# Kernel tuning notes

Measured on AMD Instinct MI355X. Metric: run time of the kernel, lower is better.

Reference implementation:

```python
import jax, jax.numpy as jnp
import numpy as np

QMIN, QMAX = -128.0, 127.0

def setup_inputs() -> dict:
    key = jax.random.key(0)
    kA, kB, ksA, ksB, kso = jax.random.split(key, 5)
    M, K, N = 8192, 4096, 4096
    # int8-valued operands (stored as int32 for portability)
    A = jax.random.randint(kA, (M, K), -128, 128, dtype=jnp.int32)
    B = jax.random.randint(kB, (N, K), -128, 128, dtype=jnp.int32)
    # strictly positive scales, typical quantization magnitudes
    scale_A = jax.random.uniform(ksA, (M,), dtype=jnp.float32, minval=0.005, maxval=0.02)
    scale_B = jax.random.uniform(ksB, (N,), dtype=jnp.float32, minval=0.005, maxval=0.02)
    scale_out = jax.random.uniform(kso, (M,), dtype=jnp.float32, minval=0.05, maxval=0.5)
    return {"A": A, "scale_A": scale_A, "B": B, "scale_B": scale_B, "scale_out": scale_out}

def reference(A, scale_A, B, scale_B, scale_out):
    # int8 GEMM with int32 accumulation: C = A @ B^T, shape (M, N)
    acc = jax.lax.dot_general(
        A, B, (((1,), (1,)), ((), ())), preferred_element_type=jnp.int32
    ).astype(jnp.float32)
    # fused three-scale dequant/requant epilogue:
    #   C_fp = acc * scale_A[m] * scale_B[n]; C_int8 = round(C_fp / scale_out[m])
    x = acc * (scale_A / scale_out)[:, None] * scale_B[None, :]
    C_int8 = jnp.clip(jnp.round(x), QMIN, QMAX).astype(jnp.int8)
    return C_int8, scale_out
```

## Files before the change

kernel.cpp:

```cpp
#include <hip/hip_runtime.h>
#include <hip/hip_bf16.h>
#include <stdint.h>

#define M_DIM 8192
#define K_DIM 4096
#define N_DIM 4096

#define BM 128
#define BN 128
#define BK 64

typedef int v4i __attribute__((ext_vector_type(4)));

__global__ void convert_pack_kernel(const int* __restrict__ A,
                                    const int* __restrict__ B,
                                    const float* __restrict__ scale_out,
                                    int8_t* __restrict__ A8,
                                    int8_t* __restrict__ B8,
                                    float* __restrict__ out_tail) {
  long gid = blockIdx.x * (long)blockDim.x + threadIdx.x;
  long stride = (long)gridDim.x * blockDim.x;

  for (long i = gid; i < M_DIM; i += stride) out_tail[i] = scale_out[i];

  const long agran = (long)M_DIM * K_DIM / 16;
  const long total = (long)(M_DIM + N_DIM) * K_DIM / 16;
  for (long g = gid; g < total; g += stride) {
    const int4* src;
    int4* dst;
    if (g < agran) {
      src = ((const int4*)A) + g * 4;
      dst = ((int4*)A8) + g;
    } else {
      long h = g - agran;
      src = ((const int4*)B) + h * 4;
      dst = ((int4*)B8) + h;
    }
    int4 a = src[0], b = src[1], c = src[2], d = src[3];
    int4 o;
    o.x = (a.x & 255) | ((a.y & 255) << 8) | ((a.z & 255) << 16) | ((a.w & 255) << 24);
    o.y = (b.x & 255) | ((b.y & 255) << 8) | ((b.z & 255) << 16) | ((b.w & 255) << 24);
    o.z = (c.x & 255) | ((c.y & 255) << 8) | ((c.z & 255) << 16) | ((c.w & 255) << 24);
    o.w = (d.x & 255) | ((d.y & 255) << 8) | ((d.z & 255) << 16) | ((d.w & 255) << 24);
    dst[0] = o;
  }
}

__global__ __launch_bounds__(256) void gemm_i8_kernel(
    const int8_t* __restrict__ A8, const int8_t* __restrict__ B8,
    const float* __restrict__ sA, const float* __restrict__ sB,
    const float* __restrict__ sO, float* __restrict__ out) {
  __shared__ int8_t lA[BM * BK];
  __shared__ int8_t lB[BN * BK];

  const int tid = threadIdx.x;
  const int wid = tid >> 6;
  const int lane = tid & 63;

  const int nwg = gridDim.x;
  const int cpx = nwg >> 3;
  const int bid = blockIdx.x;
  const int wg = (bid & 7) * cpx + (bid >> 3);
  const int tm = wg >> 5;
  const int tn = wg & 31;
  const int row0 = tm * BM;
  const int col0 = tn * BN;

  const int j = lane;
  const int koff = (((j & 3) ^ ((j >> 3) & 3)) << 4);
  const int r_lo = 16 * wid + (j >> 2);
  const int r_hi = r_lo + 64;

  const int8_t* pA0 = A8 + (size_t)(row0 + r_lo) * K_DIM + koff;
  const int8_t* pA1 = A8 + (size_t)(row0 + r_hi) * K_DIM + koff;
  const int8_t* pB0 = B8 + (size_t)(col0 + r_lo) * K_DIM + koff;
  const int8_t* pB1 = B8 + (size_t)(col0 + r_hi) * K_DIM + koff;

  int8_t* dA0 = lA + wid * 1024;
  int8_t* dA1 = lA + (wid + 4) * 1024;
  int8_t* dB0 = lB + wid * 1024;
  int8_t* dB1 = lB + (wid + 4) * 1024;

  const int fr = lane & 15;
  const int fk = lane >> 4;
  const int wr = wid >> 1;
  const int wc = wid & 1;

  int aoff[4], boff[4];
#pragma unroll
  for (int m = 0; m < 4; ++m) {
    int r = wr * 64 + m * 16 + fr;
    aoff[m] = (r * 4 + (fk ^ ((r >> 1) & 3))) * 16;
  }
#pragma unroll
  for (int n = 0; n < 4; ++n) {
    int r = wc * 64 + n * 16 + fr;
    boff[n] = (r * 4 + (fk ^ ((r >> 1) & 3))) * 16;
  }

  v4i acc[4][4];
#pragma unroll
  for (int m = 0; m < 4; ++m)
#pragma unroll
    for (int n = 0; n < 4; ++n) acc[m][n] = (v4i){0, 0, 0, 0};

  const int KSTEPS = K_DIM / BK;
  for (int kt = 0; kt < KSTEPS; ++kt) {
    __builtin_amdgcn_global_load_lds(
        (const __attribute__((address_space(1))) void*)pA0,
        (__attribute__((address_space(3))) void*)dA0, 16, 0, 0);
    __builtin_amdgcn_global_load_lds(
        (const __attribute__((address_space(1))) void*)pA1,
        (__attribute__((address_space(3))) void*)dA1, 16, 0, 0);
    __builtin_amdgcn_global_load_lds(
        (const __attribute__((address_space(1))) void*)pB0,
        (__attribute__((address_space(3))) void*)dB0, 16, 0, 0);
    __builtin_amdgcn_global_load_lds(
        (const __attribute__((address_space(1))) void*)pB1,
        (__attribute__((address_space(3))) void*)dB1, 16, 0, 0);
    pA0 += BK; pA1 += BK; pB0 += BK; pB1 += BK;

    __syncthreads();

    v4i a[4], b[4];
#pragma unroll
    for (int m = 0; m < 4; ++m) a[m] = *(const v4i*)(lA + aoff[m]);
#pragma unroll
    for (int n = 0; n < 4; ++n) b[n] = *(const v4i*)(lB + boff[n]);

#pragma unroll
    for (int m = 0; m < 4; ++m)
#pragma unroll
      for (int n = 0; n < 4; ++n)
        acc[m][n] = __builtin_amdgcn_mfma_i32_16x16x64_i8(a[m], b[n],
                                                          acc[m][n], 0, 0, 0);

    __syncthreads();
  }

  const int orow = row0 + wr * 64;
  const int ocol = col0 + wc * 64;

  float sbv[4];
#pragma unroll
  for (int n = 0; n < 4; ++n) sbv[n] = sB[ocol + n * 16 + fr];

#pragma unroll
  for (int m = 0; m < 4; ++m) {
#pragma unroll
    for (int reg = 0; reg < 4; ++reg) {
      const int grow = orow + m * 16 + fk * 4 + reg;
      const float rA = sA[grow] / sO[grow];
#pragma unroll
      for (int n = 0; n < 4; ++n) {
        float f = rintf(((float)acc[m][n][reg] * rA) * sbv[n]);
        f = fminf(127.0f, fmaxf(-128.0f, f));
        out[(size_t)grow * N_DIM + (ocol + n * 16 + fr)] = f;
      }
    }
  }
}

__global__ void gemm_naive_kernel(const int* __restrict__ A,
                                  const int* __restrict__ B,
                                  const float* __restrict__ sA,
                                  const float* __restrict__ sB,
                                  const float* __restrict__ sO,
                                  float* __restrict__ out) {
  long idx = blockIdx.x * (long)blockDim.x + threadIdx.x;
  if (idx >= (long)M_DIM * N_DIM) return;
  int m = (int)(idx / N_DIM);
  int n = (int)(idx % N_DIM);
  const int4* a = (const int4*)(A + (size_t)m * K_DIM);
  const int4* b = (const int4*)(B + (size_t)n * K_DIM);
  int acc = 0;
  for (int k = 0; k < K_DIM / 4; ++k) {
    int4 x = a[k], y = b[k];
    acc += x.x * y.x + x.y * y.y + x.z * y.z + x.w * y.w;
  }
  float f = rintf((float)acc * (sA[m] / sO[m]) * sB[n]);
  out[idx] = fminf(127.0f, fmaxf(-128.0f, f));
}

__global__ void tail_copy_kernel(const float* __restrict__ scale_out,
                                 float* __restrict__ out_tail) {
  int i = blockIdx.x * blockDim.x + threadIdx.x;
  if (i < M_DIM) out_tail[i] = scale_out[i];
}

extern "C" void kernel_launch(void* const* d_in, const int* in_sizes, int n_in,
                              void* d_out, int out_size, void* d_ws,
                              size_t ws_size, hipStream_t stream) {
  const int* A = (const int*)d_in[0];
  const float* sA = (const float*)d_in[1];
  const int* B = (const int*)d_in[2];
  const float* sB = (const float*)d_in[3];
  const float* sO = (const float*)d_in[4];
  float* out = (float*)d_out;
  float* out_tail = out + (size_t)M_DIM * N_DIM;

  const size_t need = (size_t)(M_DIM + N_DIM) * K_DIM;
  if (ws_size >= need) {
    int8_t* A8 = (int8_t*)d_ws;
    int8_t* B8 = A8 + (size_t)M_DIM * K_DIM;
    convert_pack_kernel<<<2048, 256, 0, stream>>>(A, B, sO, A8, B8, out_tail);
    gemm_i8_kernel<<<2048, 256, 0, stream>>>(A8, B8, sA, sB, sO, out);
  } else {
    tail_copy_kernel<<<(M_DIM + 255) / 256, 256, 0, stream>>>(sO, out_tail);
    long total = (long)M_DIM * N_DIM;
    int blocks = (int)((total + 255) / 256);
    gemm_naive_kernel<<<blocks, 256, 0, stream>>>(A, B, sA, sB, sO, out);
  }
}
```

Measured before the change: 470.1 us.

## Rewrite int8 GEMM as 256x256 tile, 8-wave, double-buffered phased pipeline

Replaces the 128x128x64 single-buffered GEMM with a 256x256x128 tile computed by 8 waves. The K loop runs as four phases that interleave LDS reads, async global-to-LDS staging of the next tile and MFMA bursts, with explicit barriers, waitcnt and setprio. The A/sO ratio is precomputed in the pack kernel, and packing switches to per-int4 conversion. The aim is to hide global load latency and raise data reuse per LDS byte. The cost is 128KB of LDS and a large accumulator register file, which limits occupancy to one block per CU.

After: 395.6 us. 15.9% less time.

```diff
diff --git a/kernel.cpp b/kernel.cpp
--- a/kernel.cpp
+++ b/kernel.cpp
@@ -5,157 +5,204 @@
 #define M_DIM 8192
 #define K_DIM 4096
 #define N_DIM 4096
-
-#define BM 128
-#define BN 128
-#define BK 64
+#define NT (K_DIM / 128)
 
 typedef int v4i __attribute__((ext_vector_type(4)));
 
 __global__ void convert_pack_kernel(const int* __restrict__ A,
                                     const int* __restrict__ B,
-                                    const float* __restrict__ scale_out,
-                                    int8_t* __restrict__ A8,
-                                    int8_t* __restrict__ B8,
+                                    const float* __restrict__ sA,
+                                    const float* __restrict__ sO,
+                                    int* __restrict__ A8, int* __restrict__ B8,
+                                    float* __restrict__ rAs,
                                     float* __restrict__ out_tail) {
   long gid = blockIdx.x * (long)blockDim.x + threadIdx.x;
   long stride = (long)gridDim.x * blockDim.x;
 
-  for (long i = gid; i < M_DIM; i += stride) out_tail[i] = scale_out[i];
-
-  const long agran = (long)M_DIM * K_DIM / 16;
-  const long total = (long)(M_DIM + N_DIM) * K_DIM / 16;
-  for (long g = gid; g < total; g += stride) {
-    const int4* src;
-    int4* dst;
-    if (g < agran) {
-      src = ((const int4*)A) + g * 4;
-      dst = ((int4*)A8) + g;
-    } else {
-      long h = g - agran;
-      src = ((const int4*)B) + h * 4;
-      dst = ((int4*)B8) + h;
-    }
-    int4 a = src[0], b = src[1], c = src[2], d = src[3];
-    int4 o;
-    o.x = (a.x & 255) | ((a.y & 255) << 8) | ((a.z & 255) << 16) | ((a.w & 255) << 24);
-    o.y = (b.x & 255) | ((b.y & 255) << 8) | ((b.z & 255) << 16) | ((b.w & 255) << 24);
-    o.z = (c.x & 255) | ((c.y & 255) << 8) | ((c.z & 255) << 16) | ((c.w & 255) << 24);
-    o.w = (d.x & 255) | ((d.y & 255) << 8) | ((d.z & 255) << 16) | ((d.w & 255) << 24);
-    dst[0] = o;
-  }
-}
-
-__global__ __launch_bounds__(256) void gemm_i8_kernel(
+  for (long i = gid; i < M_DIM; i += stride) {
+    float so = sO[i];
+    out_tail[i] = so;
+    rAs[i] = sA[i] / so;
+  }
+
+  const long MK4 = (long)M_DIM * (K_DIM / 4);
+  for (long i = gid; i < MK4; i += stride) {
+    int4 v = ((const int4*)A)[i];
+    A8[i] = (v.x & 255) | ((v.y & 255) << 8) | ((v.z & 255) << 16) |
+            ((v.w & 255) << 24);
+  }
+  const long NK4 = (long)N_DIM * (K_DIM / 4);
+  for (long i = gid; i < NK4; i += stride) {
+    int4 v = ((const int4*)B)[i];
+    B8[i] = (v.x & 255) | ((v.y & 255) << 8) | ((v.z & 255) << 16) |
+            ((v.w & 255) << 24);
+  }
+}
+
+__device__ __forceinline__ void stage_half(const int8_t* g, int8_t* smdst,
+                                           int rowoff, int t) {
+  const int tt = (t < NT) ? t : (NT - 1);
+  const int8_t* s = g + rowoff * K_DIM + tt * 128;
+  __builtin_amdgcn_global_load_lds(
+      (const __attribute__((address_space(1))) void*)s,
+      (__attribute__((address_space(3))) void*)smdst, 16, 0, 0);
+  __builtin_amdgcn_global_load_lds(
+      (const __attribute__((address_space(1))) void*)(s + 8 * K_DIM),
+      (__attribute__((address_space(3))) void*)(smdst + 1024), 16, 0, 0);
+}
+
+__device__ __forceinline__ void read_a4(const int8_t* smc, int ar0, int mb,
+                                        v4i a[4][2]) {
+#pragma unroll
+  for (int mm = 0; mm < 4; ++mm) {
+    a[mm][0] = *(const v4i*)(smc + (ar0 + (mb + mm) * 2048));
+    a[mm][1] = *(const v4i*)(smc + ((ar0 + (mb + mm) * 2048) ^ 64));
+  }
+}
+
+__device__ __forceinline__ void read_b2(const int8_t* smc, int br0, int nb0,
+                                        v4i b[4][2]) {
+#pragma unroll
+  for (int nn = 0; nn < 2; ++nn) {
+    b[nb0 + nn][0] = *(const v4i*)(smc + (br0 + (nb0 + nn) * 2048));
+    b[nb0 + nn][1] = *(const v4i*)(smc + ((br0 + (nb0 + nn) * 2048) ^ 64));
+  }
+}
+
+__device__ __forceinline__ void mfma16(v4i a[4][2], v4i b[4][2], v4i acc[8][4],
+                                       int am, int bn) {
+#pragma unroll
+  for (int s = 0; s < 2; ++s)
+#pragma unroll
+    for (int mm = 0; mm < 4; ++mm)
+#pragma unroll
+      for (int nn = 0; nn < 2; ++nn)
+        acc[am + mm][bn + nn] = __builtin_amdgcn_mfma_i32_16x16x64_i8(
+            a[mm][s], b[bn + nn][s], acc[am + mm][bn + nn], 0, 0, 0);
+}
+
+#define BAR() __builtin_amdgcn_s_barrier()
+#define LGKM0()                                         \
+  {                                                     \
+    asm volatile("s_waitcnt lgkmcnt(0)" ::: "memory"); \
+    __builtin_amdgcn_sched_barrier(0);                  \
+  }
+#define VM2() asm volatile("s_waitcnt vmcnt(2)" ::: "memory")
+#define SP(x) __builtin_amdgcn_s_setprio(x)
+
+__global__ __launch_bounds__(512) void gemm_i8_8phase(
     const int8_t* __restrict__ A8, const int8_t* __restrict__ B8,
-    const float* __restrict__ sA, const float* __restrict__ sB,
-    const float* __restrict__ sO, float* __restrict__ out) {
-  __shared__ int8_t lA[BM * BK];
-  __shared__ int8_t lB[BN * BK];
+    const float* __restrict__ rAs, const float* __restrict__ sB,
+    float* __restrict__ out) {
+  __shared__ int8_t sm[2][65536];
 
   const int tid = threadIdx.x;
   const int wid = tid >> 6;
-  const int lane = tid & 63;
-
-  const int nwg = gridDim.x;
-  const int cpx = nwg >> 3;
+  const int l = tid & 63;
+
   const int bid = blockIdx.x;
-  const int wg = (bid & 7) * cpx + (bid >> 3);
-  const int tm = wg >> 5;
-  const int tn = wg & 31;
-  const int row0 = tm * BM;
-  const int col0 = tn * BN;
-
-  const int j = lane;
-  const int koff = (((j & 3) ^ ((j >> 3) & 3)) << 4);
-  const int r_lo = 16 * wid + (j >> 2);
-  const int r_hi = r_lo + 64;
-
-  const int8_t* pA0 = A8 + (size_t)(row0 + r_lo) * K_DIM + koff;
-  const int8_t* pA1 = A8 + (size_t)(row0 + r_hi) * K_DIM + koff;
-  const int8_t* pB0 = B8 + (size_t)(col0 + r_lo) * K_DIM + koff;
-  const int8_t* pB1 = B8 + (size_t)(col0 + r_hi) * K_DIM + koff;
-
-  int8_t* dA0 = lA + wid * 1024;
-  int8_t* dA1 = lA + (wid + 4) * 1024;
-  int8_t* dB0 = lB + wid * 1024;
-  int8_t* dB1 = lB + (wid + 4) * 1024;
-
-  const int fr = lane & 15;
-  const int fk = lane >> 4;
-  const int wr = wid >> 1;
-  const int wc = wid & 1;
-
-  int aoff[4], boff[4];
-#pragma unroll
-  for (int m = 0; m < 4; ++m) {
-    int r = wr * 64 + m * 16 + fr;
-    aoff[m] = (r * 4 + (fk ^ ((r >> 1) & 3))) * 16;
-  }
-#pragma unroll
-  for (int n = 0; n < 4; ++n) {
-    int r = wc * 64 + n * 16 + fr;
-    boff[n] = (r * 4 + (fk ^ ((r >> 1) & 3))) * 16;
-  }
-
-  v4i acc[4][4];
-#pragma unroll
-  for (int m = 0; m < 4; ++m)
-#pragma unroll
-    for (int n = 0; n < 4; ++n) acc[m][n] = (v4i){0, 0, 0, 0};
-
-  const int KSTEPS = K_DIM / BK;
-  for (int kt = 0; kt < KSTEPS; ++kt) {
-    __builtin_amdgcn_global_load_lds(
-        (const __attribute__((address_space(1))) void*)pA0,
-        (__attribute__((address_space(3))) void*)dA0, 16, 0, 0);
-    __builtin_amdgcn_global_load_lds(
-        (const __attribute__((address_space(1))) void*)pA1,
-        (__attribute__((address_space(3))) void*)dA1, 16, 0, 0);
-    __builtin_amdgcn_global_load_lds(
-        (const __attribute__((address_space(1))) void*)pB0,
-        (__attribute__((address_space(3))) void*)dB0, 16, 0, 0);
-    __builtin_amdgcn_global_load_lds(
-        (const __attribute__((address_space(1))) void*)pB1,
-        (__attribute__((address_space(3))) void*)dB1, 16, 0, 0);
-    pA0 += BK; pA1 += BK; pB0 += BK; pB1 += BK;
-
-    __syncthreads();
-
-    v4i a[4], b[4];
-#pragma unroll
-    for (int m = 0; m < 4; ++m) a[m] = *(const v4i*)(lA + aoff[m]);
-#pragma unroll
-    for (int n = 0; n < 4; ++n) b[n] = *(const v4i*)(lB + boff[n]);
-
-#pragma unroll
-    for (int m = 0; m < 4; ++m)
-#pragma unroll
-      for (int n = 0; n < 4; ++n)
-        acc[m][n] = __builtin_amdgcn_mfma_i32_16x16x64_i8(a[m], b[n],
-                                                          acc[m][n], 0, 0, 0);
-
-    __syncthreads();
-  }
-
-  const int orow = row0 + wr * 64;
+  const int wg = (bid & 7) * (512 / 8) + (bid >> 3);
+  const int tm = wg >> 4;
+  const int tn = wg & 15;
+  const int row0 = tm * 256;
+  const int col0 = tn * 256;
+
+  const int srcChunk = ((l & 7) ^ (l >> 3)) << 4;
+  const int rowLane = l >> 3;
+  const int8_t* gA = A8 + (size_t)(row0 + rowLane) * K_DIM + srcChunk;
+  const int8_t* gB = B8 + (size_t)(col0 + rowLane) * K_DIM + srcChunk;
+
+  const int wr = wid >> 2;
+  const int wc = wid & 3;
+  const int fr = l & 15;
+  const int fk = l >> 4;
+  const int ar0 = (wr * 128 + fr) * 128 + ((fk ^ (l & 3)) << 4) +
+                  (((l >> 2) & 1) << 6);
+  const int br0 = 32768 + (wc * 64 + fr) * 128 + ((fk ^ (l & 3)) << 4) +
+                  (((l >> 2) & 1) << 6);
+
+  v4i a[4][2], b[4][2];
+  v4i acc[8][4];
+#pragma unroll
+  for (int mm = 0; mm < 8; ++mm)
+#pragma unroll
+    for (int nn = 0; nn < 4; ++nn) acc[mm][nn] = (v4i){0, 0, 0, 0};
+
+  {
+    int8_t* s0 = (int8_t*)sm[0];
+    int8_t* s1 = (int8_t*)sm[1];
+    stage_half(gA, s0 + 0 * 16384 + wid * 2048, 0 * 128 + wid * 16, 0);
+    stage_half(gA, s0 + 1 * 16384 + wid * 2048, 1 * 128 + wid * 16, 0);
+    stage_half(gB, s0 + 2 * 16384 + wid * 2048, 0 * 128 + wid * 16, 0);
+    stage_half(gB, s0 + 3 * 16384 + wid * 2048, 1 * 128 + wid * 16, 0);
+    stage_half(gA, s1 + 0 * 16384 + wid * 2048, 0 * 128 + wid * 16, 1);
+    VM2();
+    BAR();
+  }
+
+#pragma unroll 2
+  for (int T = 0; T < NT; ++T) {
+    const int cb = T & 1;
+    int8_t* smc = (int8_t*)sm[cb];
+    int8_t* smn = (int8_t*)sm[cb ^ 1];
+
+    read_a4(smc, ar0, 0, a);
+    read_b2(smc, br0, 0, b);
+    stage_half(gA, smn + 1 * 16384 + wid * 2048, 1 * 128 + wid * 16, T + 1);
+    BAR();
+    LGKM0();
+    SP(1);
+    mfma16(a, b, acc, 0, 0);
+    SP(0);
+    BAR();
+
+    read_b2(smc, br0, 2, b);
+    stage_half(gB, smn + 2 * 16384 + wid * 2048, 0 * 128 + wid * 16, T + 1);
+    BAR();
+    LGKM0();
+    SP(1);
+    mfma16(a, b, acc, 0, 2);
+    SP(0);
+    BAR();
+
+    read_a4(smc, ar0, 4, a);
+    stage_half(gB, smn + 3 * 16384 + wid * 2048, 1 * 128 + wid * 16, T + 1);
+    BAR();
+    LGKM0();
+    SP(1);
+    mfma16(a, b, acc, 4, 0);
+    SP(0);
+    BAR();
+
+    stage_half(gA, smc + 0 * 16384 + wid * 2048, 0 * 128 + wid * 16, T + 2);
+    VM2();
+    BAR();
+    SP(1);
+    mfma16(a, b, acc, 4, 2);
+    SP(0);
+    BAR();
+  }
+
+  asm volatile("s_waitcnt vmcnt(0)" ::: "memory");
+
+  const int orow = row0 + wr * 128;
   const int ocol = col0 + wc * 64;
-
   float sbv[4];
 #pragma unroll
-  for (int n = 0; n < 4; ++n) sbv[n] = sB[ocol + n * 16 + fr];
-
-#pragma unroll
-  for (int m = 0; m < 4; ++m) {
+  for (int nn = 0; nn < 4; ++nn) sbv[nn] = sB[ocol + nn * 16 + fr];
+
+#pragma unroll
+  for (int mm = 0; mm < 8; ++mm) {
 #pragma unroll
     for (int reg = 0; reg < 4; ++reg) {
-      const int grow = orow + m * 16 + fk * 4 + reg;
-      const float rA = sA[grow] / sO[grow];
-#pragma unroll
-      for (int n = 0; n < 4; ++n) {
-        float f = rintf(((float)acc[m][n][reg] * rA) * sbv[n]);
+      const int grow = orow + mm * 16 + fk * 4 + reg;
+      const float rA = rAs[grow];
+      float* op = out + (size_t)grow * N_DIM + ocol + fr;
+#pragma unroll
+      for (int nn = 0; nn < 4; ++nn) {
+        float f = rintf((float)acc[mm][nn][reg] * rA * sbv[nn]);
         f = fminf(127.0f, fmaxf(-128.0f, f));
-        out[(size_t)grow * N_DIM + (ocol + n * 16 + fr)] = f;
+        op[nn * 16] = f;
       }
     }
   }
@@ -199,12 +246,14 @@
   float* out = (float*)d_out;
   float* out_tail = out + (size_t)M_DIM * N_DIM;
 
-  const size_t need = (size_t)(M_DIM + N_DIM) * K_DIM;
+  const size_t need = (size_t)(M_DIM + N_DIM) * K_DIM + M_DIM * 4;
   if (ws_size >= need) {
     int8_t* A8 = (int8_t*)d_ws;
     int8_t* B8 = A8 + (size_t)M_DIM * K_DIM;
-    convert_pack_kernel<<<2048, 256, 0, stream>>>(A, B, sO, A8, B8, out_tail);
-    gemm_i8_kernel<<<2048, 256, 0, stream>>>(A8, B8, sA, sB, sO, out);
+    float* rAs = (float*)(B8 + (size_t)N_DIM * K_DIM);
+    convert_pack_kernel<<<2048, 256, 0, stream>>>(A, B, sA, sO, (int*)A8,
+                                                  (int*)B8, rAs, out_tail);
+    gemm_i8_8phase<<<512, 512, 0, stream>>>(A8, B8, rAs, sB, out);
   } else {
     tail_copy_kernel<<<(M_DIM + 255) / 256, 256, 0, stream>>>(sO, out_tail);
     long total = (long)M_DIM * N_DIM;
```
